# Kernel optimization log

Hardware: AMD Instinct MI355X
Metric: run time of the kernel (lower is better)

The kernel has to match this reference:

```python
import jax, jax.numpy as jnp
import numpy as np

C = 512
CQK = C // 8  # 64


def setup_inputs() -> dict:
    key = jax.random.key(0)
    ks = jax.random.split(key, 8)
    B, H, W = 16, 32, 32
    x = jax.random.normal(ks[0], (B, C, H, W), dtype=jnp.float32)
    # 1x1 conv weights stored as [out_ch, in_ch] matrices + biases
    sq = 1.0 / np.sqrt(C)
    Wq = jax.random.uniform(ks[1], (CQK, C), jnp.float32, -sq, sq)
    bq = jax.random.uniform(ks[2], (CQK,), jnp.float32, -sq, sq)
    Wk = jax.random.uniform(ks[3], (CQK, C), jnp.float32, -sq, sq)
    bk = jax.random.uniform(ks[4], (CQK,), jnp.float32, -sq, sq)
    Wv = jax.random.uniform(ks[5], (C, C), jnp.float32, -sq, sq)
    bv = jax.random.uniform(ks[6], (C,), jnp.float32, -sq, sq)
    gamma = jax.random.normal(ks[7], (1,), dtype=jnp.float32)
    return {"x": x, "Wq": Wq, "bq": bq, "Wk": Wk, "bk": bk, "Wv": Wv, "bv": bv, "gamma": gamma}


def reference(x, Wq, bq, Wk, bk, Wv, bv, gamma):
    B, Cin, H, W = x.shape
    xf = x.reshape(B, Cin, H * W)  # [B, C, N]
    # 1x1 convs == channel matmuls
    q = jnp.einsum('qc,bcn->bnq', Wq, xf) + bq[None, None, :]   # [B, N, Cqk]
    k = jnp.einsum('qc,bcn->bqn', Wk, xf) + bk[None, :, None]   # [B, Cqk, N]
    v = jnp.einsum('vc,bcn->bvn', Wv, xf) + bv[None, :, None]   # [B, C, N]
    scores = jnp.einsum('bnq,bqm->bnm', q, k)                    # [B, N, N]
    attn = jax.nn.softmax(scores, axis=-1)                       # softmax over keys
    # values @ attn^T : out[b,c,n] = sum_m v[b,c,m] * attn[b,n,m]
    attended = jnp.einsum('bvm,bnm->bvn', v, attn)               # [B, C, N]
    attended = attended.reshape(B, Cin, H, W)
    return gamma[0] * attended + x
```

## Files before the change

### kernel.cpp

```cpp
#include <hip/hip_runtime.h>
#include <stdint.h>

#define BB 16
#define CC 512
#define CQK 64
#define NN 1024

typedef __attribute__((ext_vector_type(8))) short bf16x8;
typedef __attribute__((ext_vector_type(4))) short short4v;
typedef __attribute__((ext_vector_type(8))) unsigned short ushort8;
typedef __attribute__((ext_vector_type(4))) float f32x4;

static __device__ __forceinline__ unsigned short f2bf(float f) {
  uint32_t u = __float_as_uint(f);
  u += 0x7FFFu + ((u >> 16) & 1u);
  return (unsigned short)(u >> 16);
}

static __device__ __forceinline__ void gll16(const unsigned short* g, unsigned short* l) {
  const __attribute__((address_space(1))) unsigned int* gp =
      reinterpret_cast<const __attribute__((address_space(1))) unsigned int*>(
          reinterpret_cast<uintptr_t>(g));
  __attribute__((address_space(3))) unsigned int* lp =
      reinterpret_cast<__attribute__((address_space(3))) unsigned int*>(
          (unsigned int)reinterpret_cast<uintptr_t>(l));
  __builtin_amdgcn_global_load_lds(gp, lp, 16, 0, 0);
}

__global__ __launch_bounds__(256) void k_pack_w(
    const float* __restrict__ Wq, const float* __restrict__ Wk,
    const float* __restrict__ Wv, unsigned short* __restrict__ Wall) {
  int idx = blockIdx.x * 256 + threadIdx.x;
  int e = idx * 4;
  if (e >= 640 * 512) return;
  int o = e >> 9;
  int c = e & 511;
  const float* src;
  if (o < 64)        src = Wq + (size_t)o * 512;
  else if (o < 128)  src = Wk + (size_t)(o - 64) * 512;
  else               src = Wv + (size_t)(o - 128) * 512;
  float4 v = *(const float4*)(src + c);
  short4v pk;
  pk[0] = (short)f2bf(v.x); pk[1] = (short)f2bf(v.y);
  pk[2] = (short)f2bf(v.z); pk[3] = (short)f2bf(v.w);
  *(short4v*)(Wall + e) = pk;
}

__global__ __launch_bounds__(256) void k_transpose_x(
    const float* __restrict__ x, unsigned short* __restrict__ xT) {
  __shared__ float tile[32][33];
  int b = blockIdx.z;
  int c0 = blockIdx.y * 32;
  int n0 = blockIdx.x * 32;
  int t = threadIdx.x;
  int tn = t & 31, tc = t >> 5;
  const float* xp = x + ((size_t)b * CC + c0) * NN + n0;
#pragma unroll
  for (int i = 0; i < 4; i++) {
    int c = tc + i * 8;
    tile[c][tn] = xp[(size_t)c * NN + tn];
  }
  __syncthreads();
  unsigned short* xq = xT + ((size_t)b * NN + n0) * CC + c0;
  int n = t >> 3;
  int cq = (t & 7) * 4;
  short4v pk;
#pragma unroll
  for (int k = 0; k < 4; k++) pk[k] = (short)f2bf(tile[cq + k][n]);
  *(short4v*)(&xq[(size_t)n * CC + cq]) = pk;
}

__global__ __launch_bounds__(256) void k_gemm1(
    const unsigned short* __restrict__ Wall, const unsigned short* __restrict__ xT,
    const float* __restrict__ bq, const float* __restrict__ bk,
    const float* __restrict__ bv,
    unsigned short* __restrict__ qkT, unsigned short* __restrict__ vbuf) {
  __shared__ __align__(16) unsigned short ldsA[128 * 32];
  __shared__ __align__(16) unsigned short ldsB[128 * 32];
  int b = blockIdx.z;
  int o0 = blockIdx.y * 128;
  int n0 = blockIdx.x * 128;
  int t = threadIdx.x;
  int w = t >> 6, l = t & 63;
  int wm = w & 1, wn = w >> 1;
  int lr = l & 15, lq = l >> 4;

  f32x4 acc[4][4];
#pragma unroll
  for (int i = 0; i < 4; i++)
#pragma unroll
    for (int j = 0; j < 4; j++) acc[i][j] = (f32x4){0.f, 0.f, 0.f, 0.f};

  const unsigned short* Ab = Wall + (size_t)o0 * CC;
  const unsigned short* Bb = xT + ((size_t)b * NN + n0) * CC;
  int srow = t >> 2;
  int skq = (t & 3) * 8;
  int ldsw = (t >> 6) * 512;

  for (int kt = 0; kt < CC; kt += 32) {
#pragma unroll
    for (int p = 0; p < 2; p++) {
      int r = p * 64 + srow;
      gll16(&Ab[(size_t)r * CC + kt + skq], &ldsA[p * 2048 + ldsw]);
      gll16(&Bb[(size_t)r * CC + kt + skq], &ldsB[p * 2048 + ldsw]);
    }
    __syncthreads();
    bf16x8 af[4], bfr[4];
#pragma unroll
    for (int i = 0; i < 4; i++)
      af[i] = *(const bf16x8*)(&ldsA[(wm * 64 + i * 16 + lr) * 32 + lq * 8]);
#pragma unroll
    for (int j = 0; j < 4; j++)
      bfr[j] = *(const bf16x8*)(&ldsB[(wn * 64 + j * 16 + lr) * 32 + lq * 8]);
#pragma unroll
    for (int i = 0; i < 4; i++)
#pragma unroll
      for (int j = 0; j < 4; j++)
        acc[i][j] = __builtin_amdgcn_mfma_f32_16x16x32_bf16(af[i], bfr[j], acc[i][j], 0, 0, 0);
    __syncthreads();
  }

  if (o0 == 0) {
#pragma unroll
    for (int i = 0; i < 4; i++) {
      int ob = wm * 64 + i * 16 + lq * 4;
#pragma unroll
      for (int j = 0; j < 4; j++) {
        int n = n0 + wn * 64 + j * 16 + lr;
        short4v pk;
#pragma unroll
        for (int r = 0; r < 4; r++) {
          int o = ob + r;
          float bias = (o < 64) ? bq[o] : bk[o - 64];
          pk[r] = (short)f2bf(acc[i][j][r] + bias);
        }
        *(short4v*)(&qkT[((size_t)b * NN + n) * 128 + ob]) = pk;
      }
    }
  } else {
#pragma unroll
    for (int i = 0; i < 4; i++) {
#pragma unroll
      for (int r = 0; r < 4; r++) {
        int o = o0 + wm * 64 + i * 16 + lq * 4 + r;
        int c = o - 128;
        float bias = bv[c];
#pragma unroll
        for (int j = 0; j < 4; j++) {
          int n = n0 + wn * 64 + j * 16 + lr;
          vbuf[((size_t)b * CC + c) * NN + n] = f2bf(acc[i][j][r] + bias);
        }
      }
    }
  }
}

__global__ __launch_bounds__(256) void k_attn(
    const unsigned short* __restrict__ qkT, unsigned short* __restrict__ attn) {
  __shared__ float S[16 * 1024];
  int b = blockIdx.y;
  int n0 = blockIdx.x * 16;
  int t = threadIdx.x;
  int w = t >> 6, l = t & 63;
  int lr = l & 15, lq = l >> 4;
  const unsigned short* qk = qkT + (size_t)b * NN * 128;

  bf16x8 aq[2];
#pragma unroll
  for (int ks = 0; ks < 2; ks++)
    aq[ks] = *(const bf16x8*)(&qk[(size_t)(n0 + lr) * 128 + ks * 32 + lq * 8]);

  for (int s = 0; s < 16; s++) {
    int m0 = w * 256 + s * 16;
    f32x4 a = (f32x4){0.f, 0.f, 0.f, 0.f};
#pragma unroll
    for (int ks = 0; ks < 2; ks++) {
      bf16x8 bk_ = *(const bf16x8*)(&qk[(size_t)(m0 + lr) * 128 + 64 + ks * 32 + lq * 8]);
      a = __builtin_amdgcn_mfma_f32_16x16x32_bf16(aq[ks], bk_, a, 0, 0, 0);
    }
#pragma unroll
    for (int r = 0; r < 4; r++)
      S[(lq * 4 + r) * 1024 + m0 + lr] = a[r];
  }
  __syncthreads();

#pragma unroll
  for (int rr = 0; rr < 4; rr++) {
    int row = w * 4 + rr;
    const float* Sr = &S[row * 1024];
    f32x4 v[4];
#pragma unroll
    for (int i = 0; i < 4; i++) v[i] = *(const f32x4*)(&Sr[l * 16 + i * 4]);
    float mx = -1e30f;
#pragma unroll
    for (int i = 0; i < 4; i++)
#pragma unroll
      for (int j = 0; j < 4; j++) mx = fmaxf(mx, v[i][j]);
#pragma unroll
    for (int d = 1; d < 64; d <<= 1) mx = fmaxf(mx, __shfl_xor(mx, d, 64));
    float sum = 0.f;
#pragma unroll
    for (int i = 0; i < 4; i++)
#pragma unroll
      for (int j = 0; j < 4; j++) {
        float e = __expf(v[i][j] - mx);
        v[i][j] = e;
        sum += e;
      }
#pragma unroll
    for (int d = 1; d < 64; d <<= 1) sum += __shfl_xor(sum, d, 64);
    float inv = 1.0f / sum;
    ushort8 p0, p1;
#pragma unroll
    for (int j = 0; j < 4; j++) {
      p0[j]     = f2bf(v[0][j] * inv);
      p0[4 + j] = f2bf(v[1][j] * inv);
      p1[j]     = f2bf(v[2][j] * inv);
      p1[4 + j] = f2bf(v[3][j] * inv);
    }
    unsigned short* ap = attn + ((size_t)b * NN + n0 + row) * NN + l * 16;
    *(ushort8*)(ap) = p0;
    *(ushort8*)(ap + 8) = p1;
  }
}

__global__ __launch_bounds__(256) void k_gemm3(
    const unsigned short* __restrict__ vbuf, const unsigned short* __restrict__ attn,
    const float* __restrict__ x, const float* __restrict__ gamma,
    float* __restrict__ out) {
  __shared__ __align__(16) unsigned short ldsA[128 * 32];
  __shared__ __align__(16) unsigned short ldsB[128 * 32];
  int b = blockIdx.z;
  int c0 = blockIdx.y * 128;
  int n0 = blockIdx.x * 128;
  int t = threadIdx.x;
  int w = t >> 6, l = t & 63;
  int wm = w & 1, wn = w >> 1;
  int lr = l & 15, lq = l >> 4;

  f32x4 acc[4][4];
#pragma unroll
  for (int i = 0; i < 4; i++)
#pragma unroll
    for (int j = 0; j < 4; j++) acc[i][j] = (f32x4){0.f, 0.f, 0.f, 0.f};

  const unsigned short* Ab = vbuf + ((size_t)b * CC + c0) * NN;
  const unsigned short* Bb = attn + ((size_t)b * NN + n0) * NN;
  int srow = t >> 2;
  int skq = (t & 3) * 8;
  int ldsw = (t >> 6) * 512;

  for (int kt = 0; kt < NN; kt += 32) {
#pragma unroll
    for (int p = 0; p < 2; p++) {
      int r = p * 64 + srow;
      gll16(&Ab[(size_t)r * NN + kt + skq], &ldsA[p * 2048 + ldsw]);
      gll16(&Bb[(size_t)r * NN + kt + skq], &ldsB[p * 2048 + ldsw]);
    }
    __syncthreads();
    bf16x8 af[4], bfr[4];
#pragma unroll
    for (int i = 0; i < 4; i++)
      af[i] = *(const bf16x8*)(&ldsA[(wm * 64 + i * 16 + lr) * 32 + lq * 8]);
#pragma unroll
    for (int j = 0; j < 4; j++)
      bfr[j] = *(const bf16x8*)(&ldsB[(wn * 64 + j * 16 + lr) * 32 + lq * 8]);
#pragma unroll
    for (int i = 0; i < 4; i++)
#pragma unroll
      for (int j = 0; j < 4; j++)
        acc[i][j] = __builtin_amdgcn_mfma_f32_16x16x32_bf16(af[i], bfr[j], acc[i][j], 0, 0, 0);
    __syncthreads();
  }

  float g = gamma[0];
#pragma unroll
  for (int i = 0; i < 4; i++) {
#pragma unroll
    for (int r = 0; r < 4; r++) {
      int c = c0 + wm * 64 + i * 16 + lq * 4 + r;
#pragma unroll
      for (int j = 0; j < 4; j++) {
        int n = n0 + wn * 64 + j * 16 + lr;
        size_t idx = ((size_t)b * CC + c) * NN + n;
        out[idx] = g * acc[i][j][r] + x[idx];
      }
    }
  }
}

extern "C" void kernel_launch(void* const* d_in, const int* in_sizes, int n_in,
                              void* d_out, int out_size, void* d_ws, size_t ws_size,
                              hipStream_t stream) {
  (void)in_sizes; (void)n_in; (void)out_size; (void)ws_size;
  const float* x     = (const float*)d_in[0];
  const float* Wq    = (const float*)d_in[1];
  const float* bq    = (const float*)d_in[2];
  const float* Wk    = (const float*)d_in[3];
  const float* bk    = (const float*)d_in[4];
  const float* Wv    = (const float*)d_in[5];
  const float* bv    = (const float*)d_in[6];
  const float* gamma = (const float*)d_in[7];
  float* out = (float*)d_out;

  char* ws = (char*)d_ws;
  unsigned short* Wall = (unsigned short*)(ws);
  unsigned short* xT   = (unsigned short*)(ws + 655360);
  unsigned short* qkT  = (unsigned short*)(ws + 655360 + 16777216);
  unsigned short* vbuf = (unsigned short*)(ws + 655360 + 16777216 + 4194304);
  unsigned short* attn = (unsigned short*)(ws + 655360 + 16777216 + 4194304 + 16777216);

  k_pack_w<<<dim3(320), dim3(256), 0, stream>>>(Wq, Wk, Wv, Wall);
  k_transpose_x<<<dim3(NN / 32, CC / 32, BB), dim3(256), 0, stream>>>(x, xT);
  k_gemm1<<<dim3(NN / 128, 640 / 128, BB), dim3(256), 0, stream>>>(Wall, xT, bq, bk, bv, qkT, vbuf);
  k_attn<<<dim3(NN / 16, BB), dim3(256), 0, stream>>>(qkT, attn);
  k_gemm3<<<dim3(NN / 128, CC / 128, BB), dim3(256), 0, stream>>>(vbuf, attn, x, gamma, out);
}
```

Baseline: 180.9 us.

## Fuse softmax with attention-value GEMM, keep probabilities in LDS

Merges the softmax kernel and the attention-times-values GEMM into one kernel. Unnormalized probabilities are stored as bf16 in shared memory with a padded stride, and the 1/sum normalization is applied in the epilogue. This removes the 32MB bf16 attention matrix write and read and one kernel launch. The cost is that each 16-query block now streams the full per-batch V (512x1024 bf16) straight from global memory with no LDS reuse, across 1024 blocks, and the output stores are less coalesced.

```diff
diff --git a/kernel.cpp b/kernel.cpp
--- a/kernel.cpp
+++ b/kernel.cpp
@@ -155,9 +155,15 @@
   }
 }
 
-__global__ __launch_bounds__(256) void k_attn(
-    const unsigned short* __restrict__ qkT, unsigned short* __restrict__ attn) {
-  __shared__ float S[16 * 1024];
+#define PSTRIDE 1032
+__global__ __launch_bounds__(256) void k_attn_pv(
+    const unsigned short* __restrict__ qkT, const unsigned short* __restrict__ vbuf,
+    const float* __restrict__ x, const float* __restrict__ gamma,
+    float* __restrict__ out) {
+  __shared__ __align__(16) float Sbuf[16 * 1024];
+  unsigned short* P = (unsigned short*)Sbuf;
+  float* invs = (float*)((char*)Sbuf + 16 * PSTRIDE * 2);
+
   int b = blockIdx.y;
   int n0 = blockIdx.x * 16;
   int t = threadIdx.x;
@@ -169,33 +175,36 @@
 #pragma unroll
   for (int ks = 0; ks < 2; ks++)
     aq[ks] = *(const bf16x8*)(&qk[(size_t)(n0 + lr) * 128 + ks * 32 + lq * 8]);
-
   for (int s = 0; s < 16; s++) {
     int m0 = w * 256 + s * 16;
     f32x4 a = (f32x4){0.f, 0.f, 0.f, 0.f};
 #pragma unroll
     for (int ks = 0; ks < 2; ks++) {
-      bf16x8 bk_ = *(const bf16x8*)(&qk[(size_t)(m0 + lr) * 128 + 64 + ks * 32 + lq * 8]);
-      a = __builtin_amdgcn_mfma_f32_16x16x32_bf16(aq[ks], bk_, a, 0, 0, 0);
+      bf16x8 kf = *(const bf16x8*)(&qk[(size_t)(m0 + lr) * 128 + 64 + ks * 32 + lq * 8]);
+      a = __builtin_amdgcn_mfma_f32_16x16x32_bf16(aq[ks], kf, a, 0, 0, 0);
     }
 #pragma unroll
     for (int r = 0; r < 4; r++)
-      S[(lq * 4 + r) * 1024 + m0 + lr] = a[r];
-  }
+      Sbuf[(lq * 4 + r) * 1024 + m0 + lr] = a[r];
+  }
+  __syncthreads();
+
+  f32x4 v[4][4];
+#pragma unroll
+  for (int rr = 0; rr < 4; rr++)
+#pragma unroll
+    for (int i = 0; i < 4; i++)
+      v[rr][i] = *(const f32x4*)(&Sbuf[(w * 4 + rr) * 1024 + l * 16 + i * 4]);
   __syncthreads();
 
 #pragma unroll
   for (int rr = 0; rr < 4; rr++) {
     int row = w * 4 + rr;
-    const float* Sr = &S[row * 1024];
-    f32x4 v[4];
-#pragma unroll
-    for (int i = 0; i < 4; i++) v[i] = *(const f32x4*)(&Sr[l * 16 + i * 4]);
     float mx = -1e30f;
 #pragma unroll
     for (int i = 0; i < 4; i++)
 #pragma unroll
-      for (int j = 0; j < 4; j++) mx = fmaxf(mx, v[i][j]);
+      for (int j = 0; j < 4; j++) mx = fmaxf(mx, v[rr][i][j]);
 #pragma unroll
     for (int d = 1; d < 64; d <<= 1) mx = fmaxf(mx, __shfl_xor(mx, d, 64));
     float sum = 0.f;
@@ -203,88 +212,48 @@
     for (int i = 0; i < 4; i++)
 #pragma unroll
       for (int j = 0; j < 4; j++) {
-        float e = __expf(v[i][j] - mx);
-        v[i][j] = e;
+        float e = __expf(v[rr][i][j] - mx);
+        v[rr][i][j] = e;
         sum += e;
       }
 #pragma unroll
     for (int d = 1; d < 64; d <<= 1) sum += __shfl_xor(sum, d, 64);
-    float inv = 1.0f / sum;
     ushort8 p0, p1;
 #pragma unroll
     for (int j = 0; j < 4; j++) {
-      p0[j]     = f2bf(v[0][j] * inv);
-      p0[4 + j] = f2bf(v[1][j] * inv);
-      p1[j]     = f2bf(v[2][j] * inv);
-      p1[4 + j] = f2bf(v[3][j] * inv);
-    }
-    unsigned short* ap = attn + ((size_t)b * NN + n0 + row) * NN + l * 16;
-    *(ushort8*)(ap) = p0;
-    *(ushort8*)(ap + 8) = p1;
-  }
-}
-
-__global__ __launch_bounds__(256) void k_gemm3(
-    const unsigned short* __restrict__ vbuf, const unsigned short* __restrict__ attn,
-    const float* __restrict__ x, const float* __restrict__ gamma,
-    float* __restrict__ out) {
-  __shared__ __align__(16) unsigned short ldsA[128 * 32];
-  __shared__ __align__(16) unsigned short ldsB[128 * 32];
-  int b = blockIdx.z;
-  int c0 = blockIdx.y * 128;
-  int n0 = blockIdx.x * 128;
-  int t = threadIdx.x;
-  int w = t >> 6, l = t & 63;
-  int wm = w & 1, wn = w >> 1;
-  int lr = l & 15, lq = l >> 4;
-
-  f32x4 acc[4][4];
-#pragma unroll
-  for (int i = 0; i < 4; i++)
-#pragma unroll
-    for (int j = 0; j < 4; j++) acc[i][j] = (f32x4){0.f, 0.f, 0.f, 0.f};
-
-  const unsigned short* Ab = vbuf + ((size_t)b * CC + c0) * NN;
-  const unsigned short* Bb = attn + ((size_t)b * NN + n0) * NN;
-  int srow = t >> 2;
-  int skq = (t & 3) * 8;
-  int ldsw = (t >> 6) * 512;
-
-  for (int kt = 0; kt < NN; kt += 32) {
-#pragma unroll
-    for (int p = 0; p < 2; p++) {
-      int r = p * 64 + srow;
-      gll16(&Ab[(size_t)r * NN + kt + skq], &ldsA[p * 2048 + ldsw]);
-      gll16(&Bb[(size_t)r * NN + kt + skq], &ldsB[p * 2048 + ldsw]);
-    }
-    __syncthreads();
-    bf16x8 af[4], bfr[4];
-#pragma unroll
-    for (int i = 0; i < 4; i++)
-      af[i] = *(const bf16x8*)(&ldsA[(wm * 64 + i * 16 + lr) * 32 + lq * 8]);
-#pragma unroll
-    for (int j = 0; j < 4; j++)
-      bfr[j] = *(const bf16x8*)(&ldsB[(wn * 64 + j * 16 + lr) * 32 + lq * 8]);
-#pragma unroll
-    for (int i = 0; i < 4; i++)
-#pragma unroll
-      for (int j = 0; j < 4; j++)
-        acc[i][j] = __builtin_amdgcn_mfma_f32_16x16x32_bf16(af[i], bfr[j], acc[i][j], 0, 0, 0);
-    __syncthreads();
+      p0[j]     = f2bf(v[rr][0][j]);
+      p0[4 + j] = f2bf(v[rr][1][j]);
+      p1[j]     = f2bf(v[rr][2][j]);
+      p1[4 + j] = f2bf(v[rr][3][j]);
+    }
+    *(ushort8*)(&P[row * PSTRIDE + l * 16]) = p0;
+    *(ushort8*)(&P[row * PSTRIDE + l * 16 + 8]) = p1;
+    if (l == 0) invs[row] = 1.0f / sum;
+  }
+  __syncthreads();
+
+  const unsigned short* Vb = vbuf + ((size_t)b * CC + w * 128) * NN;
+  f32x4 acc[8];
+#pragma unroll
+  for (int ci = 0; ci < 8; ci++) acc[ci] = (f32x4){0.f, 0.f, 0.f, 0.f};
+  for (int mk = 0; mk < NN; mk += 32) {
+    bf16x8 bf_ = *(const bf16x8*)(&P[lr * PSTRIDE + mk + lq * 8]);
+#pragma unroll
+    for (int ci = 0; ci < 8; ci++) {
+      bf16x8 af = *(const bf16x8*)(&Vb[(size_t)(ci * 16 + lr) * NN + mk + lq * 8]);
+      acc[ci] = __builtin_amdgcn_mfma_f32_16x16x32_bf16(af, bf_, acc[ci], 0, 0, 0);
+    }
   }
 
   float g = gamma[0];
-#pragma unroll
-  for (int i = 0; i < 4; i++) {
+  float iv = invs[lr];
+#pragma unroll
+  for (int ci = 0; ci < 8; ci++) {
 #pragma unroll
     for (int r = 0; r < 4; r++) {
-      int c = c0 + wm * 64 + i * 16 + lq * 4 + r;
-#pragma unroll
-      for (int j = 0; j < 4; j++) {
-        int n = n0 + wn * 64 + j * 16 + lr;
-        size_t idx = ((size_t)b * CC + c) * NN + n;
-        out[idx] = g * acc[i][j][r] + x[idx];
-      }
+      int c = w * 128 + ci * 16 + lq * 4 + r;
+      size_t idx = ((size_t)b * CC + c) * NN + n0 + lr;
+      out[idx] = g * acc[ci][r] * iv + x[idx];
     }
   }
 }
@@ -308,11 +277,9 @@
   unsigned short* xT   = (unsigned short*)(ws + 655360);
   unsigned short* qkT  = (unsigned short*)(ws + 655360 + 16777216);
   unsigned short* vbuf = (unsigned short*)(ws + 655360 + 16777216 + 4194304);
-  unsigned short* attn = (unsigned short*)(ws + 655360 + 16777216 + 4194304 + 16777216);
 
   k_pack_w<<<dim3(320), dim3(256), 0, stream>>>(Wq, Wk, Wv, Wall);
   k_transpose_x<<<dim3(NN / 32, CC / 32, BB), dim3(256), 0, stream>>>(x, xT);
   k_gemm1<<<dim3(NN / 128, 640 / 128, BB), dim3(256), 0, stream>>>(Wall, xT, bq, bk, bv, qkT, vbuf);
-  k_attn<<<dim3(NN / 16, BB), dim3(256), 0, stream>>>(qkT, attn);
-  k_gemm3<<<dim3(NN / 128, CC / 128, BB), dim3(256), 0, stream>>>(vbuf, attn, x, gamma, out);
-}
+  k_attn_pv<<<dim3(NN / 16, BB), dim3(256), 0, stream>>>(qkT, vbuf, x, gamma, out);
+}
```

Result: slower. 299.3 us (+65.5%).
